# Kernel tuning notes

Measured on AMD Instinct MI355X. Metric: run time of the kernel, lower is better.

Reference implementation:

```python
import jax, jax.numpy as jnp
import numpy as np


def setup_inputs() -> dict:
    key = jax.random.key(0)
    ks = jax.random.split(key, 20)
    B, T, E, U, D, O = 64, 2048, 256, 256, 256, 32000
    s = lambda k, shp, fan: (jax.random.normal(k, shp, jnp.float32) * (1.0 / np.sqrt(fan)))
    return {
        'inputs': jax.random.normal(ks[0], (B, D), jnp.float32),
        'stm': jax.random.normal(ks[1], (B, U), jnp.float32),
        'x_seq': jax.random.normal(ks[2], (B, T, E), jnp.float32),
        'V_a': s(ks[3], (U + E,), U + E),
        'W_a': s(ks[4], (U + E, U + E), U + E),
        'W_r': s(ks[5], (D, U), D), 'U_r': s(ks[6], (U, U), U), 'C_r': s(ks[7], (E, U), E), 'b_r': jnp.zeros((U,), jnp.float32),
        'W_z': s(ks[8], (D, U), D), 'U_z': s(ks[9], (U, U), U), 'C_z': s(ks[10], (E, U), E), 'b_z': jnp.zeros((U,), jnp.float32),
        'W_p': s(ks[11], (D, U), D), 'U_p': s(ks[12], (U, U), U), 'C_p': s(ks[13], (E, U), E), 'b_p': jnp.zeros((U,), jnp.float32),
        'W_o': s(ks[14], (D, O), D), 'U_o': s(ks[15], (U, O), U), 'C_o': s(ks[16], (E, O), E), 'b_o': jnp.zeros((O,), jnp.float32),
    }


def reference(inputs, stm, x_seq, V_a, W_a,
              W_r, U_r, C_r, b_r,
              W_z, U_z, C_z, b_z,
              W_p, U_p, C_p, b_p,
              W_o, U_o, C_o, b_o):
    B, T, E = x_seq.shape
    U = stm.shape[-1]
    # Bahdanau additive attention: concat repeated state with encoder seq
    _stm = jnp.broadcast_to(stm[:, None, :], (B, T, U))          # [B,T,U]
    cat = jnp.concatenate([_stm, x_seq], axis=-1)                 # [B,T,U+E]
    et = jnp.einsum('btc,c->bt', jnp.tanh(jnp.einsum('btc,cd->btd', cat, W_a)), V_a)
    at = jax.nn.softmax(et, axis=1)                               # exp / sum over T
    context = jnp.einsum('bt,bte->be', at, x_seq)                 # [B,E]
    # GRU-style gates conditioned on input, previous state, and context
    rt = jax.nn.sigmoid(inputs @ W_r + stm @ U_r + context @ C_r + b_r)
    zt = jax.nn.sigmoid(inputs @ W_z + stm @ U_z + context @ C_z + b_z)
    s_tp = jnp.tanh(inputs @ W_p + (rt * stm) @ U_p + context @ C_p + b_p)
    st = (1.0 - zt) * stm + zt * s_tp                             # new state [B,U]
    output = jax.nn.softmax(inputs @ W_o + stm @ U_o + context @ C_o + b_o, axis=-1)  # [B,O]
    return output, st
```

## Files before the change

### kernel.cpp

```cpp
#include <hip/hip_runtime.h>
#include <hip/hip_bf16.h>

#define B_ 64
#define T_ 2048
#define E_ 256
#define U_ 256
#define O_ 32000
#define UE_ 512

typedef __attribute__((ext_vector_type(8))) short bf16x8;
typedef __attribute__((ext_vector_type(4))) float f32x4;

__device__ __forceinline__ unsigned short f2bf(float f){
  __hip_bfloat16 h = __float2bfloat16(f);
  return __builtin_bit_cast(unsigned short, h);
}
__device__ __forceinline__ unsigned pk2bf(float a, float b){
  return (unsigned)f2bf(a) | ((unsigned)f2bf(b) << 16);
}
__device__ __forceinline__ bf16x8 pack8(const float* v0, const float* v1){
  float4 x = *(const float4*)v0;
  float4 y = *(const float4*)v1;
  uint4 pk;
  pk.x = pk2bf(x.x, x.y); pk.y = pk2bf(x.z, x.w);
  pk.z = pk2bf(y.x, y.y); pk.w = pk2bf(y.z, y.w);
  return __builtin_bit_cast(bf16x8, pk);
}
__device__ __forceinline__ float ftanh(float x){
  float e = __expf(2.0f*x);
  return 1.0f - 2.0f/(e + 1.0f);
}
__device__ __forceinline__ float fsig(float x){
  return 1.0f/(1.0f + __expf(-x));
}

__global__ __launch_bounds__(256)
void prep_kernel(const float* __restrict__ Wa, const float* __restrict__ stm,
                 unsigned short* __restrict__ bpack, float* __restrict__ sp){
  if (blockIdx.x < 64){
    int idx = blockIdx.x*256 + threadIdx.x;
    int n = idx & 511;
    int ktg = idx >> 9;
    int erow = ktg * 8;
    unsigned short o[8];
#pragma unroll
    for (int i = 0; i < 8; ++i)
      o[i] = f2bf(Wa[(256 + erow + i)*512 + n]);
    uint4 v;
    v.x = (unsigned)o[0] | ((unsigned)o[1] << 16);
    v.y = (unsigned)o[2] | ((unsigned)o[3] << 16);
    v.z = (unsigned)o[4] | ((unsigned)o[5] << 16);
    v.w = (unsigned)o[6] | ((unsigned)o[7] << 16);
    ((uint4*)bpack)[idx] = v;
  } else {
    int tid = threadIdx.x;
    int w = tid >> 6, l = tid & 63, c = l & 15, g = l >> 4;
    int n0 = (blockIdx.x - 64)*64 + w*16;
    f32x4 zero = {0.f,0.f,0.f,0.f};
    f32x4 acc[4];
#pragma unroll
    for (int mt = 0; mt < 4; ++mt) acc[mt] = zero;
#pragma unroll
    for (int ks = 0; ks < 8; ++ks){
      int kg = ks*32 + 8*g;
      bf16x8 a[4];
#pragma unroll
      for (int mt = 0; mt < 4; ++mt){
        const float* ap = stm + (mt*16 + c)*256 + kg;
        a[mt] = pack8(ap, ap + 4);
      }
      const float* bpt = Wa + (size_t)kg*512 + n0 + c;
      float bv[8];
#pragma unroll
      for (int i = 0; i < 8; ++i) bv[i] = bpt[(size_t)i*512];
      uint4 pk;
      pk.x = pk2bf(bv[0], bv[1]); pk.y = pk2bf(bv[2], bv[3]);
      pk.z = pk2bf(bv[4], bv[5]); pk.w = pk2bf(bv[6], bv[7]);
      bf16x8 bfr = __builtin_bit_cast(bf16x8, pk);
#pragma unroll
      for (int mt = 0; mt < 4; ++mt)
        acc[mt] = __builtin_amdgcn_mfma_f32_16x16x32_bf16(a[mt], bfr, acc[mt], 0, 0, 0);
    }
#pragma unroll
    for (int mt = 0; mt < 4; ++mt)
#pragma unroll
      for (int r = 0; r < 4; ++r){
        int m = mt*16 + 4*g + r;
        sp[m*512 + n0 + c] = acc[mt][r];
      }
  }
}

__global__ __launch_bounds__(512, 4)
void et_kernel(const float* __restrict__ xseq, const unsigned short* __restrict__ bpack,
               const float* __restrict__ va, const float* __restrict__ sp,
               float* __restrict__ et){
  __shared__ __align__(16) uint4 sA4[2048];
  __shared__ float sVa[512];
  __shared__ float sSp[512];
  __shared__ float sEt[8][64];
  int tid = threadIdx.x;
  int w = tid >> 6, l = tid & 63, c = l & 15, g = l >> 4;
  int m0 = blockIdx.x * 64;
  int b  = m0 >> 11;

  const float4* x4 = (const float4*)xseq + (size_t)m0 * 64;
  uint2* sA2 = (uint2*)sA4;
#pragma unroll
  for (int i = 0; i < 8; ++i){
    int p = i*512 + tid;
    int row = p >> 6, kq = p & 63;
    float4 v = x4[row*64 + kq];
    uint2 u;
    u.x = pk2bf(v.x, v.y);
    u.y = pk2bf(v.z, v.w);
    int s = ((row>>4)*8 + (kq>>3))*64 + ((kq>>1)&3)*16 + (row&15);
    sA2[(s ^ ((s>>4)&7))*2 + (kq&1)] = u;
  }
  sVa[tid] = va[tid];
  sSp[tid] = sp[b*512 + tid];
  __syncthreads();

  f32x4 zero = {0.f, 0.f, 0.f, 0.f};
  f32x4 acc[4][4];
#pragma unroll
  for (int mt = 0; mt < 4; ++mt)
#pragma unroll
    for (int tc = 0; tc < 4; ++tc) acc[mt][tc] = zero;

  const bf16x8* bp = (const bf16x8*)bpack;
#pragma unroll
  for (int ks = 0; ks < 8; ++ks){
    bf16x8 aw[4], bx[4];
    int bbase = (ks*4 + g)*512 + w*64 + c;
#pragma unroll
    for (int mt = 0; mt < 4; ++mt)
      aw[mt] = bp[bbase + mt*16];
#pragma unroll
    for (int tc = 0; tc < 4; ++tc){
      int idx = (tc*8 + ks)*64 + l;
      bx[tc] = *(const bf16x8*)&sA4[idx ^ ((idx>>4)&7)];
    }
#pragma unroll
    for (int mt = 0; mt < 4; ++mt)
#pragma unroll
      for (int tc = 0; tc < 4; ++tc)
        acc[mt][tc] = __builtin_amdgcn_mfma_f32_16x16x32_bf16(aw[mt], bx[tc], acc[mt][tc], 0, 0, 0);
  }

  float p[4] = {0.f, 0.f, 0.f, 0.f};
#pragma unroll
  for (int mt = 0; mt < 4; ++mt){
    int nb = w*64 + mt*16 + 4*g;
    float4 vav = *(const float4*)&sVa[nb];
    float4 spv = *(const float4*)&sSp[nb];
#pragma unroll
    for (int tc = 0; tc < 4; ++tc){
#pragma unroll
      for (int r = 0; r < 4; ++r){
        float vv = acc[mt][tc][r] + ((const float*)&spv)[r];
        p[tc] += ((const float*)&vav)[r] * ftanh(vv);
      }
    }
  }
#pragma unroll
  for (int tc = 0; tc < 4; ++tc){
    p[tc] += __shfl_xor(p[tc], 16, 64);
    p[tc] += __shfl_xor(p[tc], 32, 64);
  }
  if (l < 16){
#pragma unroll
    for (int tc = 0; tc < 4; ++tc)
      sEt[w][tc*16 + c] = p[tc];
  }
  __syncthreads();
  if (tid < 64){
    float e = 0.f;
#pragma unroll
    for (int ww = 0; ww < 8; ++ww) e += sEt[ww][tid];
    et[m0 + tid] = e;
  }
}

__global__ void at_kernel(const float* __restrict__ et, float* __restrict__ at){
  __shared__ float red[4];
  __shared__ float red2[4];
  int b = blockIdx.x, tid = threadIdx.x;
  float v[8];
#pragma unroll
  for (int i = 0; i < 8; ++i) v[i] = et[b*2048 + i*256 + tid];
  float m = v[0];
#pragma unroll
  for (int i = 1; i < 8; ++i) m = fmaxf(m, v[i]);
#pragma unroll
  for (int off = 1; off < 64; off <<= 1) m = fmaxf(m, __shfl_xor(m, off, 64));
  int wv = tid >> 6;
  if ((tid & 63) == 0) red[wv] = m;
  __syncthreads();
  m = fmaxf(fmaxf(red[0], red[1]), fmaxf(red[2], red[3]));
  float e[8]; float s = 0.f;
#pragma unroll
  for (int i = 0; i < 8; ++i){ e[i] = __expf(v[i] - m); s += e[i]; }
#pragma unroll
  for (int off = 1; off < 64; off <<= 1) s += __shfl_xor(s, off, 64);
  if ((tid & 63) == 0) red2[wv] = s;
  __syncthreads();
  s = red2[0] + red2[1] + red2[2] + red2[3];
  float inv = 1.0f / s;
#pragma unroll
  for (int i = 0; i < 8; ++i) at[b*2048 + i*256 + tid] = e[i] * inv;
}

__global__ void ctxpart_kernel(const float* __restrict__ at, const float* __restrict__ xseq,
                               float* __restrict__ cp){
  __shared__ float s_at[256];
  int ch = blockIdx.x;
  int b  = blockIdx.y;
  int e  = threadIdx.x;
  int t0 = ch * 256;
  s_at[e] = at[b*2048 + t0 + e];
  __syncthreads();
  float acc = 0.f;
  const float* xp = xseq + ((size_t)(b*2048 + t0))*256 + e;
#pragma unroll 4
  for (int tt = 0; tt < 256; ++tt)
    acc += s_at[tt] * xp[(size_t)tt * 256];
  cp[(b*8 + ch)*256 + e] = acc;
}

__global__ void ctx_x1_kernel(const float* __restrict__ cp, const float* __restrict__ inputs,
                              const float* __restrict__ stm,
                              unsigned short* __restrict__ X1bf){
  int b = blockIdx.x, e = threadIdx.x;
  float s = 0.f;
#pragma unroll
  for (int c = 0; c < 8; ++c) s += cp[(b*8 + c)*256 + e];
  X1bf[b*768 + e]        = f2bf(inputs[b*256 + e]);
  X1bf[b*768 + 256 + e]  = f2bf(stm[b*256 + e]);
  X1bf[b*768 + 512 + e]  = f2bf(s);
}

__global__ __launch_bounds__(256)
void gates1_kernel(const unsigned short* __restrict__ X1bf, const float* __restrict__ stm,
                   const float* __restrict__ Wr, const float* __restrict__ Ur,
                   const float* __restrict__ Cr, const float* __restrict__ brr,
                   const float* __restrict__ Wz, const float* __restrict__ Uz,
                   const float* __restrict__ Cz, const float* __restrict__ bzz,
                   const float* __restrict__ Wp, const float* __restrict__ Cp,
                   const float* __restrict__ bpp,
                   float* __restrict__ rs, float* __restrict__ ztb, float* __restrict__ pic){
  int tid = threadIdx.x;
  int w = tid >> 6, l = tid & 63, c = l & 15, g = l >> 4;
  int n0 = blockIdx.x*64 + w*16;
  int gate = n0 >> 8;
  int col0 = n0 & 255;
  const float* W0; const float* W1; const float* W2; const float* bias;
  if (gate == 0){ W0 = Wr; W1 = Ur; W2 = Cr; bias = brr; }
  else if (gate == 1){ W0 = Wz; W1 = Uz; W2 = Cz; bias = bzz; }
  else { W0 = Wp; W1 = nullptr; W2 = Cp; bias = bpp; }

  f32x4 zero = {0.f,0.f,0.f,0.f};
  f32x4 acc[4];
#pragma unroll
  for (int mt = 0; mt < 4; ++mt) acc[mt] = zero;

#pragma unroll
  for (int ph = 0; ph < 3; ++ph){
    const float* src = (ph == 0) ? W0 : (ph == 1) ? W1 : W2;
    if (src == nullptr) continue;
#pragma unroll
    for (int ks = 0; ks < 8; ++ks){
      int kg = ks*32 + 8*g;
      bf16x8 a[4];
#pragma unroll
      for (int mt = 0; mt < 4; ++mt)
        a[mt] = *(const bf16x8*)&X1bf[(mt*16 + c)*768 + ph*256 + kg];
      const float* bpt = src + (size_t)kg*256 + col0 + c;
      float bv[8];
#pragma unroll
      for (int i = 0; i < 8; ++i) bv[i] = bpt[(size_t)i*256];
      uint4 pk;
      pk.x = pk2bf(bv[0], bv[1]); pk.y = pk2bf(bv[2], bv[3]);
      pk.z = pk2bf(bv[4], bv[5]); pk.w = pk2bf(bv[6], bv[7]);
      bf16x8 bfr = __builtin_bit_cast(bf16x8, pk);
#pragma unroll
      for (int mt = 0; mt < 4; ++mt)
        acc[mt] = __builtin_amdgcn_mfma_f32_16x16x32_bf16(a[mt], bfr, acc[mt], 0, 0, 0);
    }
  }

  int n = col0 + c;
  float bi = bias[n];
#pragma unroll
  for (int mt = 0; mt < 4; ++mt)
#pragma unroll
    for (int r = 0; r < 4; ++r){
      int m = mt*16 + 4*g + r;
      float pre = acc[mt][r] + bi;
      if (gate == 0)      rs[m*256 + n]  = fsig(pre) * stm[m*256 + n];
      else if (gate == 1) ztb[m*256 + n] = fsig(pre);
      else                pic[m*256 + n] = pre;
    }
}

__global__ __launch_bounds__(256)
void gates2_kernel(const float* __restrict__ rs, const float* __restrict__ Up,
                   const float* __restrict__ pic, const float* __restrict__ ztb,
                   const float* __restrict__ stm, float* __restrict__ stout){
  int tid = threadIdx.x;
  int w = tid >> 6, l = tid & 63, c = l & 15, g = l >> 4;
  int n0 = blockIdx.x*64 + w*16;
  f32x4 zero = {0.f,0.f,0.f,0.f};
  f32x4 acc[4];
#pragma unroll
  for (int mt = 0; mt < 4; ++mt) acc[mt] = zero;
#pragma unroll
  for (int ks = 0; ks < 8; ++ks){
    int kg = ks*32 + 8*g;
    bf16x8 a[4];
#pragma unroll
    for (int mt = 0; mt < 4; ++mt){
      const float* ap = rs + (mt*16 + c)*256 + kg;
      a[mt] = pack8(ap, ap + 4);
    }
    const float* bpt = Up + (size_t)kg*256 + n0 + c;
    float bv[8];
#pragma unroll
    for (int i = 0; i < 8; ++i) bv[i] = bpt[(size_t)i*256];
    uint4 pk;
    pk.x = pk2bf(bv[0], bv[1]); pk.y = pk2bf(bv[2], bv[3]);
    pk.z = pk2bf(bv[4], bv[5]); pk.w = pk2bf(bv[6], bv[7]);
    bf16x8 bfr = __builtin_bit_cast(bf16x8, pk);
#pragma unroll
    for (int mt = 0; mt < 4; ++mt)
      acc[mt] = __builtin_amdgcn_mfma_f32_16x16x32_bf16(a[mt], bfr, acc[mt], 0, 0, 0);
  }
#pragma unroll
  for (int mt = 0; mt < 4; ++mt)
#pragma unroll
    for (int r = 0; r < 4; ++r){
      int m = mt*16 + 4*g + r;
      int o = m*256 + n0 + c;
      float ap = pic[o] + acc[mt][r];
      float z = ztb[o];
      stout[o] = (1.f - z)*stm[o] + z*ftanh(ap);
    }
}

__global__ __launch_bounds__(512)
void logits_mfma_kernel(const unsigned short* __restrict__ X1bf,
                        const float* __restrict__ Wo, const float* __restrict__ Uo,
                        const float* __restrict__ Co, const float* __restrict__ boo,
                        float* __restrict__ outl){
  __shared__ float sAcc[16][4][64];
  int tid = threadIdx.x;
  int w = tid >> 6, l = tid & 63, c = l & 15, g = l >> 4;
  int wc = w & 3;
  int kh = w >> 2;
  int n0 = blockIdx.x*64 + wc*16;
  f32x4 zero = {0.f,0.f,0.f,0.f};
  f32x4 acc[4];
#pragma unroll
  for (int mt = 0; mt < 4; ++mt) acc[mt] = zero;

#pragma unroll
  for (int ph = 0; ph < 3; ++ph){
    const float* src = (ph == 0) ? Wo : (ph == 1) ? Uo : Co;
#pragma unroll
    for (int kss = 0; kss < 4; ++kss){
      int ks = 2*kss + kh;
      int kg = ph*256 + ks*32 + 8*g;
      bf16x8 a[4];
#pragma unroll
      for (int mt = 0; mt < 4; ++mt)
        a[mt] = *(const bf16x8*)&X1bf[(mt*16 + c)*768 + kg];
      const float* bpt = src + (size_t)(ks*32 + 8*g)*32000 + n0 + c;
      float bv[8];
#pragma unroll
      for (int i = 0; i < 8; ++i) bv[i] = bpt[(size_t)i*32000];
      uint4 pk;
      pk.x = pk2bf(bv[0], bv[1]);
      pk.y = pk2bf(bv[2], bv[3]);
      pk.z = pk2bf(bv[4], bv[5]);
      pk.w = pk2bf(bv[6], bv[7]);
      bf16x8 bfr = __builtin_bit_cast(bf16x8, pk);
#pragma unroll
      for (int mt = 0; mt < 4; ++mt)
        acc[mt] = __builtin_amdgcn_mfma_f32_16x16x32_bf16(a[mt], bfr, acc[mt], 0, 0, 0);
    }
  }

  if (kh == 1){
#pragma unroll
    for (int mt = 0; mt < 4; ++mt)
#pragma unroll
      for (int r = 0; r < 4; ++r)
        sAcc[mt*4 + r][wc][l] = acc[mt][r];
  }
  __syncthreads();
  if (kh == 0){
    float bias = boo[n0 + c];
#pragma unroll
    for (int mt = 0; mt < 4; ++mt)
#pragma unroll
      for (int r = 0; r < 4; ++r){
        int m = mt*16 + 4*g + r;
        float vv = acc[mt][r] + sAcc[mt*4 + r][wc][l] + bias;
        outl[(size_t)m*32000 + n0 + c] = vv;
      }
  }
}

__global__ void sm_part_kernel(const float* __restrict__ logits, float* __restrict__ part){
  __shared__ float red[4];
  __shared__ float red2[4];
  int bid = blockIdx.x;
  int b = bid >> 3, ch = bid & 7;
  int base = b*32000 + ch*4000;
  int tid = threadIdx.x;
  float v[16];
#pragma unroll
  for (int i = 0; i < 16; ++i){
    int idx = i*256 + tid;
    v[i] = (idx < 4000) ? logits[base + idx] : -INFINITY;
  }
  float m = v[0];
#pragma unroll
  for (int i = 1; i < 16; ++i) m = fmaxf(m, v[i]);
#pragma unroll
  for (int off = 1; off < 64; off <<= 1) m = fmaxf(m, __shfl_xor(m, off, 64));
  int wv = tid >> 6;
  if ((tid & 63) == 0) red[wv] = m;
  __syncthreads();
  m = fmaxf(fmaxf(red[0], red[1]), fmaxf(red[2], red[3]));
  float s = 0.f;
#pragma unroll
  for (int i = 0; i < 16; ++i) s += __expf(v[i] - m);
#pragma unroll
  for (int off = 1; off < 64; off <<= 1) s += __shfl_xor(s, off, 64);
  if ((tid & 63) == 0) red2[wv] = s;
  __syncthreads();
  if (tid == 0){
    float st = red2[0] + red2[1] + red2[2] + red2[3];
    part[bid*2]     = m;
    part[bid*2 + 1] = st;
  }
}

__global__ void sm_norm_kernel(float* __restrict__ logits, const float* __restrict__ part){
  int bid = blockIdx.x;
  int b = bid >> 3, ch = bid & 7;
  int base = b*32000 + ch*4000;
  int tid = threadIdx.x;
  float M = -INFINITY;
#pragma unroll
  for (int cc = 0; cc < 8; ++cc) M = fmaxf(M, part[(b*8 + cc)*2]);
  float S = 0.f;
#pragma unroll
  for (int cc = 0; cc < 8; ++cc) S += part[(b*8 + cc)*2 + 1] * __expf(part[(b*8 + cc)*2] - M);
  float inv = 1.0f / S;
#pragma unroll
  for (int i = 0; i < 16; ++i){
    int idx = i*256 + tid;
    if (idx < 4000){
      int o = base + idx;
      logits[o] = __expf(logits[o] - M) * inv;
    }
  }
}

extern "C" void kernel_launch(void* const* d_in, const int* in_sizes, int n_in,
                              void* d_out, int out_size, void* d_ws, size_t ws_size,
                              hipStream_t stream) {
  const float* inputs = (const float*)d_in[0];
  const float* stm    = (const float*)d_in[1];
  const float* xseq   = (const float*)d_in[2];
  const float* Va     = (const float*)d_in[3];
  const float* Wa     = (const float*)d_in[4];
  const float* Wr = (const float*)d_in[5];
  const float* Ur = (const float*)d_in[6];
  const float* Cr = (const float*)d_in[7];
  const float* br = (const float*)d_in[8];
  const float* Wz = (const float*)d_in[9];
  const float* Uz = (const float*)d_in[10];
  const float* Cz = (const float*)d_in[11];
  const float* bz = (const float*)d_in[12];
  const float* Wp = (const float*)d_in[13];
  const float* Up = (const float*)d_in[14];
  const float* Cp = (const float*)d_in[15];
  const float* bp = (const float*)d_in[16];
  const float* Wo = (const float*)d_in[17];
  const float* Uo = (const float*)d_in[18];
  const float* Co = (const float*)d_in[19];
  const float* bo = (const float*)d_in[20];

  float* out   = (float*)d_out;
  float* stout = out + (size_t)B_*O_;

  float* wsf = (float*)d_ws;
  unsigned short* bpack = (unsigned short*)d_ws;
  float* sp   = wsf + 65536;
  float* et   = wsf + 98304;
  float* at   = wsf + 229376;
  float* cp   = wsf + 360448;
  unsigned short* X1bf = (unsigned short*)(wsf + 491520);
  float* part = wsf + 516096;
  float* rs   = wsf + 517120;
  float* ztb  = wsf + 533504;
  float* pic  = wsf + 549888;

  prep_kernel<<<72, 256, 0, stream>>>(Wa, stm, bpack, sp);
  et_kernel<<<2048, 512, 0, stream>>>(xseq, bpack, Va, sp, et);
  at_kernel<<<64, 256, 0, stream>>>(et, at);
  ctxpart_kernel<<<dim3(8, 64), 256, 0, stream>>>(at, xseq, cp);
  ctx_x1_kernel<<<64, 256, 0, stream>>>(cp, inputs, stm, X1bf);
  gates1_kernel<<<12, 256, 0, stream>>>(X1bf, stm, Wr, Ur, Cr, br,
                                        Wz, Uz, Cz, bz, Wp, Cp, bp,
                                        rs, ztb, pic);
  gates2_kernel<<<4, 256, 0, stream>>>(rs, Up, pic, ztb, stm, stout);
  logits_mfma_kernel<<<500, 512, 0, stream>>>(X1bf, Wo, Uo, Co, bo, out);
  sm_part_kernel<<<512, 256, 0, stream>>>(out, part);
  sm_norm_kernel<<<512, 256, 0, stream>>>(out, part);
}
```

Baseline: 177.1 us.

## Split et_kernel output columns across block pairs and double-buffer two row tiles

```diff
diff --git a/kernel.cpp b/kernel.cpp
--- a/kernel.cpp
+++ b/kernel.cpp
@@ -7,6 +7,7 @@
 #define U_ 256
 #define O_ 32000
 #define UE_ 512
+#define MROWS 131072
 
 typedef __attribute__((ext_vector_type(8))) short bf16x8;
 typedef __attribute__((ext_vector_type(4))) float f32x4;
@@ -91,104 +92,133 @@
   }
 }
 
-__global__ __launch_bounds__(512, 4)
+__global__ __launch_bounds__(512)
 void et_kernel(const float* __restrict__ xseq, const unsigned short* __restrict__ bpack,
                const float* __restrict__ va, const float* __restrict__ sp,
-               float* __restrict__ et){
-  __shared__ __align__(16) uint4 sA4[2048];
+               float* __restrict__ etp){
+  __shared__ __align__(16) uint4 sA4[2][2048];
   __shared__ float sVa[512];
   __shared__ float sSp[512];
-  __shared__ float sEt[8][64];
+  __shared__ float sEt[2][8][64];
   int tid = threadIdx.x;
   int w = tid >> 6, l = tid & 63, c = l & 15, g = l >> 4;
-  int m0 = blockIdx.x * 64;
+  int ch = blockIdx.x & 1;
+  int rp = blockIdx.x >> 1;
+  int m0 = rp * 128;
   int b  = m0 >> 11;
 
-  const float4* x4 = (const float4*)xseq + (size_t)m0 * 64;
-  uint2* sA2 = (uint2*)sA4;
-#pragma unroll
-  for (int i = 0; i < 8; ++i){
-    int p = i*512 + tid;
-    int row = p >> 6, kq = p & 63;
-    float4 v = x4[row*64 + kq];
-    uint2 u;
-    u.x = pk2bf(v.x, v.y);
-    u.y = pk2bf(v.z, v.w);
-    int s = ((row>>4)*8 + (kq>>3))*64 + ((kq>>1)&3)*16 + (row&15);
-    sA2[(s ^ ((s>>4)&7))*2 + (kq&1)] = u;
+  const float4* x4 = (const float4*)xseq;
+  const bf16x8* bp = (const bf16x8*)bpack;
+
+  float4 f[8];
+  {
+    size_t base = (size_t)m0 * 64;
+#pragma unroll
+    for (int i = 0; i < 8; ++i) f[i] = x4[base + i*512 + tid];
   }
   sVa[tid] = va[tid];
   sSp[tid] = sp[b*512 + tid];
-  __syncthreads();
-
-  f32x4 zero = {0.f, 0.f, 0.f, 0.f};
-  f32x4 acc[4][4];
-#pragma unroll
-  for (int mt = 0; mt < 4; ++mt)
-#pragma unroll
-    for (int tc = 0; tc < 4; ++tc) acc[mt][tc] = zero;
-
-  const bf16x8* bp = (const bf16x8*)bpack;
-#pragma unroll
-  for (int ks = 0; ks < 8; ++ks){
-    bf16x8 aw[4], bx[4];
-    int bbase = (ks*4 + g)*512 + w*64 + c;
-#pragma unroll
-    for (int mt = 0; mt < 4; ++mt)
-      aw[mt] = bp[bbase + mt*16];
+
+#pragma unroll
+  for (int i = 0; i < 8; ++i){
+    int p = i*512 + tid, row = p >> 6, kq = p & 63;
+    uint2 u;
+    u.x = pk2bf(f[i].x, f[i].y);
+    u.y = pk2bf(f[i].z, f[i].w);
+    int s = ((row>>4)*8 + (kq>>3))*64 + ((kq>>1)&3)*16 + (row&15);
+    ((uint2*)sA4[0])[(s ^ ((s>>4)&7))*2 + (kq&1)] = u;
+  }
+  {
+    size_t base = (size_t)(m0 + 64) * 64;
+#pragma unroll
+    for (int i = 0; i < 8; ++i) f[i] = x4[base + i*512 + tid];
+  }
+  __syncthreads();
+
+#pragma unroll
+  for (int t = 0; t < 2; ++t){
+    f32x4 zero = {0.f,0.f,0.f,0.f};
+    f32x4 acc[2][4];
+#pragma unroll
+    for (int mt = 0; mt < 2; ++mt)
+#pragma unroll
+      for (int tc = 0; tc < 4; ++tc) acc[mt][tc] = zero;
+
+#pragma unroll
+    for (int ks = 0; ks < 8; ++ks){
+      bf16x8 aw[2], bx[4];
+      int bbase = (ks*4 + g)*512 + ch*256 + w*32 + c;
+      aw[0] = bp[bbase];
+      aw[1] = bp[bbase + 16];
+#pragma unroll
+      for (int tc = 0; tc < 4; ++tc){
+        int idx = (tc*8 + ks)*64 + l;
+        bx[tc] = *(const bf16x8*)&sA4[t][idx ^ ((idx>>4)&7)];
+      }
+#pragma unroll
+      for (int mt = 0; mt < 2; ++mt)
+#pragma unroll
+        for (int tc = 0; tc < 4; ++tc)
+          acc[mt][tc] = __builtin_amdgcn_mfma_f32_16x16x32_bf16(aw[mt], bx[tc], acc[mt][tc], 0, 0, 0);
+    }
+
+    float p[4] = {0.f, 0.f, 0.f, 0.f};
+#pragma unroll
+    for (int mt = 0; mt < 2; ++mt){
+      int nb = ch*256 + w*32 + mt*16 + 4*g;
+      float4 vav = *(const float4*)&sVa[nb];
+      float4 spv = *(const float4*)&sSp[nb];
+#pragma unroll
+      for (int tc = 0; tc < 4; ++tc){
+#pragma unroll
+        for (int r = 0; r < 4; ++r){
+          float vv = acc[mt][tc][r] + ((const float*)&spv)[r];
+          p[tc] += ((const float*)&vav)[r] * ftanh(vv);
+        }
+      }
+    }
 #pragma unroll
     for (int tc = 0; tc < 4; ++tc){
-      int idx = (tc*8 + ks)*64 + l;
-      bx[tc] = *(const bf16x8*)&sA4[idx ^ ((idx>>4)&7)];
-    }
-#pragma unroll
-    for (int mt = 0; mt < 4; ++mt)
+      p[tc] += __shfl_xor(p[tc], 16, 64);
+      p[tc] += __shfl_xor(p[tc], 32, 64);
+    }
+    if (l < 16){
 #pragma unroll
       for (int tc = 0; tc < 4; ++tc)
-        acc[mt][tc] = __builtin_amdgcn_mfma_f32_16x16x32_bf16(aw[mt], bx[tc], acc[mt][tc], 0, 0, 0);
-  }
-
-  float p[4] = {0.f, 0.f, 0.f, 0.f};
-#pragma unroll
-  for (int mt = 0; mt < 4; ++mt){
-    int nb = w*64 + mt*16 + 4*g;
-    float4 vav = *(const float4*)&sVa[nb];
-    float4 spv = *(const float4*)&sSp[nb];
-#pragma unroll
-    for (int tc = 0; tc < 4; ++tc){
-#pragma unroll
-      for (int r = 0; r < 4; ++r){
-        float vv = acc[mt][tc][r] + ((const float*)&spv)[r];
-        p[tc] += ((const float*)&vav)[r] * ftanh(vv);
+        sEt[t][w][tc*16 + c] = p[tc];
+    }
+
+    if (t == 0){
+#pragma unroll
+      for (int i = 0; i < 8; ++i){
+        int pq = i*512 + tid, row = pq >> 6, kq = pq & 63;
+        uint2 u;
+        u.x = pk2bf(f[i].x, f[i].y);
+        u.y = pk2bf(f[i].z, f[i].w);
+        int s = ((row>>4)*8 + (kq>>3))*64 + ((kq>>1)&3)*16 + (row&15);
+        ((uint2*)sA4[1])[(s ^ ((s>>4)&7))*2 + (kq&1)] = u;
       }
     }
-  }
-#pragma unroll
-  for (int tc = 0; tc < 4; ++tc){
-    p[tc] += __shfl_xor(p[tc], 16, 64);
-    p[tc] += __shfl_xor(p[tc], 32, 64);
-  }
-  if (l < 16){
-#pragma unroll
-    for (int tc = 0; tc < 4; ++tc)
-      sEt[w][tc*16 + c] = p[tc];
-  }
-  __syncthreads();
-  if (tid < 64){
-    float e = 0.f;
-#pragma unroll
-    for (int ww = 0; ww < 8; ++ww) e += sEt[ww][tid];
-    et[m0 + tid] = e;
-  }
-}
-
-__global__ void at_kernel(const float* __restrict__ et, float* __restrict__ at){
+    __syncthreads();
+    if (tid < 64){
+      float e = 0.f;
+#pragma unroll
+      for (int ww = 0; ww < 8; ++ww) e += sEt[t][ww][tid];
+      etp[(size_t)ch*MROWS + m0 + t*64 + tid] = e;
+    }
+  }
+}
+
+__global__ void at_kernel(const float* __restrict__ etp, float* __restrict__ at){
   __shared__ float red[4];
   __shared__ float red2[4];
   int b = blockIdx.x, tid = threadIdx.x;
   float v[8];
 #pragma unroll
-  for (int i = 0; i < 8; ++i) v[i] = et[b*2048 + i*256 + tid];
+  for (int i = 0; i < 8; ++i){
+    int o = b*2048 + i*256 + tid;
+    v[i] = etp[o] + etp[MROWS + o];
+  }
   float m = v[0];
 #pragma unroll
   for (int i = 1; i < 8; ++i) m = fmaxf(m, v[i]);
@@ -500,18 +530,18 @@
   float* wsf = (float*)d_ws;
   unsigned short* bpack = (unsigned short*)d_ws;
   float* sp   = wsf + 65536;
-  float* et   = wsf + 98304;
-  float* at   = wsf + 229376;
-  float* cp   = wsf + 360448;
-  unsigned short* X1bf = (unsigned short*)(wsf + 491520);
-  float* part = wsf + 516096;
-  float* rs   = wsf + 517120;
-  float* ztb  = wsf + 533504;
-  float* pic  = wsf + 549888;
+  float* etp  = wsf + 98304;
+  float* at   = wsf + 360448;
+  float* cp   = wsf + 491520;
+  unsigned short* X1bf = (unsigned short*)(wsf + 622592);
+  float* part = wsf + 647168;
+  float* rs   = wsf + 648192;
+  float* ztb  = wsf + 664576;
+  float* pic  = wsf + 680960;
 
   prep_kernel<<<72, 256, 0, stream>>>(Wa, stm, bpack, sp);
-  et_kernel<<<2048, 512, 0, stream>>>(xseq, bpack, Va, sp, et);
-  at_kernel<<<64, 256, 0, stream>>>(et, at);
+  et_kernel<<<2048, 512, 0, stream>>>(xseq, bpack, Va, sp, etp);
+  at_kernel<<<64, 256, 0, stream>>>(etp, at);
   ctxpart_kernel<<<dim3(8, 64), 256, 0, stream>>>(at, xseq, cp);
   ctx_x1_kernel<<<64, 256, 0, stream>>>(cp, inputs, stm, X1bf);
   gates1_kernel<<<12, 256, 0, stream>>>(X1bf, stm, Wr, Ur, Cr, br,
```

Result: slower. 208.8 us (+17.9%).

## Fuse attention softmax and context into score kernel with online-softmax partials

Applied to the files above, without the earlier changes.

```diff
diff --git a/kernel.cpp b/kernel.cpp
--- a/kernel.cpp
+++ b/kernel.cpp
@@ -92,13 +92,14 @@
 }
 
 __global__ __launch_bounds__(512, 4)
-void et_kernel(const float* __restrict__ xseq, const unsigned short* __restrict__ bpack,
-               const float* __restrict__ va, const float* __restrict__ sp,
-               float* __restrict__ et){
+void et_flash_kernel(const float* __restrict__ xseq, const unsigned short* __restrict__ bpack,
+                     const float* __restrict__ va, const float* __restrict__ sp,
+                     float* __restrict__ msbuf, float* __restrict__ uctxp){
   __shared__ __align__(16) uint4 sA4[2048];
   __shared__ float sVa[512];
   __shared__ float sSp[512];
   __shared__ float sEt[8][64];
+  __shared__ float sE[64];
   int tid = threadIdx.x;
   int w = tid >> 6, l = tid & 63, c = l & 15, g = l >> 4;
   int m0 = blockIdx.x * 64;
@@ -174,70 +175,64 @@
       sEt[w][tc*16 + c] = p[tc];
   }
   __syncthreads();
+
   if (tid < 64){
     float e = 0.f;
 #pragma unroll
     for (int ww = 0; ww < 8; ++ww) e += sEt[ww][tid];
-    et[m0 + tid] = e;
-  }
-}
-
-__global__ void at_kernel(const float* __restrict__ et, float* __restrict__ at){
-  __shared__ float red[4];
-  __shared__ float red2[4];
-  int b = blockIdx.x, tid = threadIdx.x;
-  float v[8];
-#pragma unroll
-  for (int i = 0; i < 8; ++i) v[i] = et[b*2048 + i*256 + tid];
-  float m = v[0];
-#pragma unroll
-  for (int i = 1; i < 8; ++i) m = fmaxf(m, v[i]);
-#pragma unroll
-  for (int off = 1; off < 64; off <<= 1) m = fmaxf(m, __shfl_xor(m, off, 64));
-  int wv = tid >> 6;
-  if ((tid & 63) == 0) red[wv] = m;
+    float m = e;
+#pragma unroll
+    for (int off = 1; off < 64; off <<= 1) m = fmaxf(m, __shfl_xor(m, off, 64));
+    float ex = __expf(e - m);
+    float s = ex;
+#pragma unroll
+    for (int off = 1; off < 64; off <<= 1) s += __shfl_xor(s, off, 64);
+    sE[tid] = ex;
+    if (tid == 0){
+      msbuf[blockIdx.x*2]     = m;
+      msbuf[blockIdx.x*2 + 1] = s;
+    }
+  }
   __syncthreads();
-  m = fmaxf(fmaxf(red[0], red[1]), fmaxf(red[2], red[3]));
-  float e[8]; float s = 0.f;
-#pragma unroll
-  for (int i = 0; i < 8; ++i){ e[i] = __expf(v[i] - m); s += e[i]; }
-#pragma unroll
-  for (int off = 1; off < 64; off <<= 1) s += __shfl_xor(s, off, 64);
-  if ((tid & 63) == 0) red2[wv] = s;
-  __syncthreads();
-  s = red2[0] + red2[1] + red2[2] + red2[3];
-  float inv = 1.0f / s;
-#pragma unroll
-  for (int i = 0; i < 8; ++i) at[b*2048 + i*256 + tid] = e[i] * inv;
-}
-
-__global__ void ctxpart_kernel(const float* __restrict__ at, const float* __restrict__ xseq,
-                               float* __restrict__ cp){
-  __shared__ float s_at[256];
-  int ch = blockIdx.x;
-  int b  = blockIdx.y;
-  int e  = threadIdx.x;
-  int t0 = ch * 256;
-  s_at[e] = at[b*2048 + t0 + e];
-  __syncthreads();
-  float acc = 0.f;
-  const float* xp = xseq + ((size_t)(b*2048 + t0))*256 + e;
-#pragma unroll 4
-  for (int tt = 0; tt < 256; ++tt)
-    acc += s_at[tt] * xp[(size_t)tt * 256];
-  cp[(b*8 + ch)*256 + e] = acc;
-}
-
-__global__ void ctx_x1_kernel(const float* __restrict__ cp, const float* __restrict__ inputs,
-                              const float* __restrict__ stm,
+
+  {
+    int e = tid & 255, th = tid >> 8;
+    int ks = e >> 5, gg = (e >> 3) & 3, ii = e & 7;
+    const unsigned short* sU = (const unsigned short*)sA4;
+    float a0 = 0.f;
+#pragma unroll
+    for (int tt = 0; tt < 32; ++tt){
+      int t = th*32 + tt;
+      int mt = t >> 4, cc = t & 15;
+      int slt = (mt*8 + ks)*64 + gg*16 + cc;
+      unsigned short hv = sU[(size_t)(slt ^ ((slt>>4)&7))*8 + ii];
+      float xv = __builtin_bit_cast(float, ((unsigned)hv) << 16);
+      a0 += sE[t] * xv;
+    }
+    uctxp[((size_t)blockIdx.x*2 + th)*256 + e] = a0;
+  }
+}
+
+__global__ void ctx_x1_kernel(const float* __restrict__ msbuf, const float* __restrict__ uctxp,
+                              const float* __restrict__ inputs, const float* __restrict__ stm,
                               unsigned short* __restrict__ X1bf){
   int b = blockIdx.x, e = threadIdx.x;
-  float s = 0.f;
-#pragma unroll
-  for (int c = 0; c < 8; ++c) s += cp[(b*8 + c)*256 + e];
+  float M = -INFINITY;
+#pragma unroll 4
+  for (int j = 0; j < 32; ++j) M = fmaxf(M, msbuf[(32*b + j)*2]);
+  float S = 0.f;
+  float acc = 0.f;
+#pragma unroll 4
+  for (int j = 0; j < 32; ++j){
+    float wj = __expf(msbuf[(32*b + j)*2] - M);
+    S += msbuf[(32*b + j)*2 + 1] * wj;
+    size_t base = ((size_t)(32*b + j)*2)*256 + e;
+    acc += (uctxp[base] + uctxp[base + 256]) * wj;
+  }
+  float ctx = acc / S;
   X1bf[b*768 + e]        = f2bf(inputs[b*256 + e]);
   X1bf[b*768 + 256 + e]  = f2bf(stm[b*256 + e]);
-  X1bf[b*768 + 512 + e]  = f2bf(s);
+  X1bf[b*768 + 512 + e]  = f2bf(ctx);
 }
 
 __global__ __launch_bounds__(256)
@@ -499,21 +494,18 @@
 
   float* wsf = (float*)d_ws;
   unsigned short* bpack = (unsigned short*)d_ws;
-  float* sp   = wsf + 65536;
-  float* et   = wsf + 98304;
-  float* at   = wsf + 229376;
-  float* cp   = wsf + 360448;
-  unsigned short* X1bf = (unsigned short*)(wsf + 491520);
-  float* part = wsf + 516096;
-  float* rs   = wsf + 517120;
-  float* ztb  = wsf + 533504;
-  float* pic  = wsf + 549888;
+  float* sp    = wsf + 65536;
+  float* msbuf = wsf + 98304;
+  float* uctxp = wsf + 102400;
+  unsigned short* X1bf = (unsigned short*)(wsf + 1150976);
+  float* part  = wsf + 1175552;
+  float* rs    = wsf + 1176576;
+  float* ztb   = wsf + 1192960;
+  float* pic   = wsf + 1209344;
 
   prep_kernel<<<72, 256, 0, stream>>>(Wa, stm, bpack, sp);
-  et_kernel<<<2048, 512, 0, stream>>>(xseq, bpack, Va, sp, et);
-  at_kernel<<<64, 256, 0, stream>>>(et, at);
-  ctxpart_kernel<<<dim3(8, 64), 256, 0, stream>>>(at, xseq, cp);
-  ctx_x1_kernel<<<64, 256, 0, stream>>>(cp, inputs, stm, X1bf);
+  et_flash_kernel<<<2048, 512, 0, stream>>>(xseq, bpack, Va, sp, msbuf, uctxp);
+  ctx_x1_kernel<<<64, 256, 0, stream>>>(msbuf, uctxp, inputs, stm, X1bf);
   gates1_kernel<<<12, 256, 0, stream>>>(X1bf, stm, Wr, Ur, Cr, br,
                                         Wz, Uz, Cz, bz, Wp, Cp, bp,
                                         rs, ztb, pic);
```

Result: faster. 163.7 us (-7.5%).
